# Optimization experiments

Hardware: AMD Instinct MI355X
Metric: run time of the kernel (lower is better)

The kernel has to match this reference:

```python
import jax, jax.numpy as jnp
import numpy as np

N, D, H, E = 50000, 64, 4, 400000
LN_EPS = 1e-5


def setup_inputs() -> dict:
    key = jax.random.key(0)
    ks = jax.random.split(key, 8)
    x = jax.random.normal(ks[0], (N, D), dtype=jnp.float32)
    edge_index = jax.random.randint(ks[1], (2, E), 0, N, dtype=jnp.int64)
    # nn.Linear(dim, dim*heads, bias=False): weight shape (H*D, D)
    W_lin = jax.random.normal(ks[2], (H * D, D), dtype=jnp.float32) * (1.0 / np.sqrt(D))
    attn_src = jax.random.normal(ks[3], (H, D), dtype=jnp.float32) * 0.1
    attn_dst = jax.random.normal(ks[4], (H, D), dtype=jnp.float32) * 0.1
    # nn.Linear(dim*heads, dim): weight (D, H*D), bias (D,)
    W_out = jax.random.normal(ks[5], (D, H * D), dtype=jnp.float32) * (1.0 / np.sqrt(H * D))
    b_out = jnp.zeros((D,), dtype=jnp.float32)
    ln_g = jnp.ones((D,), dtype=jnp.float32)
    ln_b = jnp.zeros((D,), dtype=jnp.float32)
    return {"x": x, "edge_index": edge_index, "W_lin": W_lin,
            "attn_src": attn_src, "attn_dst": attn_dst,
            "W_out": W_out, "b_out": b_out, "ln_g": ln_g, "ln_b": ln_b}


def reference(x, edge_index, W_lin, attn_src, attn_dst, W_out, b_out, ln_g, ln_b):
    n = x.shape[0]
    i, j = edge_index[0], edge_index[1]  # dst, src node ids per edge
    xh = (x @ W_lin.T).reshape(n, H, D)                 # [N,H,D]
    # per-node attention contributions (equivalent to per-edge dot in source)
    s_dst = jnp.einsum('nhd,hd->nh', xh, attn_dst)      # [N,H]
    s_src = jnp.einsum('nhd,hd->nh', xh, attn_src)      # [N,H]
    alpha = jax.nn.leaky_relu(s_dst[i] + s_src[j], 0.2) # [E,H]
    alpha_exp = jnp.exp(alpha)                          # source uses raw exp (no max-shift)
    denom = jax.ops.segment_sum(alpha_exp, i, num_segments=n)  # [N,H]
    attn = alpha_exp / (denom[i] + 1e-9)                # [E,H]
    msg = attn[:, :, None] * xh[j]                      # [E,H,D]
    out = jax.ops.segment_sum(msg, i, num_segments=n)   # [N,H,D]
    out = out.reshape(n, H * D) @ W_out.T + b_out       # [N,D]
    y = jax.nn.elu(out) + x
    mu = jnp.mean(y, axis=-1, keepdims=True)
    var = jnp.mean(jnp.square(y - mu), axis=-1, keepdims=True)
    return (y - mu) * jax.lax.rsqrt(var + LN_EPS) * ln_g + ln_b
```

## Files before the change

kernel.cpp:

```cpp
#include <hip/hip_runtime.h>

#define N_NODES 50000
#define DIM     64
#define HEADS   4
#define NEDGES  400000
#define HD      256
#define MAXDEG  32
#define NPREP   2048
#define ZSTRIDE 264

#define USE_DOT2 1

typedef _Float16 half2v __attribute__((ext_vector_type(2)));
typedef _Float16 half4v __attribute__((ext_vector_type(4)));
typedef _Float16 half8v __attribute__((ext_vector_type(8)));
typedef float    f32x4  __attribute__((ext_vector_type(4)));

union EU { int2 i2; half4v h; };
union HU { unsigned int u; half2v h; };

__device__ __forceinline__ half2v h2cast(unsigned int u) { HU c; c.u = u; return c.h; }

#if USE_DOT2
#define DOT2(a, b, c) __builtin_amdgcn_fdot2((a), (b), (c), false)
#else
__device__ __forceinline__ float DOT2(half2v a, half2v b, float c) {
    return fmaf((float)a[1], (float)b[1], fmaf((float)a[0], (float)b[0], c));
}
#endif

__global__ __launch_bounds__(256) void k_prep(
    const float* __restrict__ x,
    const float* __restrict__ W_lin,
    const float* __restrict__ attn_src,
    const float* __restrict__ attn_dst,
    const float* __restrict__ W_out,
    const int* __restrict__ ei,
    _Float16* __restrict__ G2T,
    _Float16* __restrict__ x16,
    float* __restrict__ S,
    int* __restrict__ cnt,
    unsigned short* __restrict__ bucketJ)
{
    __shared__ float weffsh[8][68];
    const int b = blockIdx.x, t = threadIdx.x;
    const int base = b * 32;

    const size_t e0 = (size_t)base * DIM + (size_t)t * 8;
    const bool do_x = (e0 + 8 <= (size_t)N_NODES * DIM);
    float4 u = {0.f, 0.f, 0.f, 0.f}, v = {0.f, 0.f, 0.f, 0.f};
    if (do_x) {
        u = *(const float4*)(x + e0);
        v = *(const float4*)(x + e0 + 4);
    }

    for (int e = b * 256 + t; e < NEDGES; e += NPREP * 256) {
        const int i = ei[e];
        const int j = ei[NEDGES + e];
        const int slot = atomicAdd(&cnt[i], 1);
        if (slot < MAXDEG)
            bucketJ[(size_t)i * MAXDEG + slot] = (unsigned short)j;
    }

    for (int id = t; id < 512; id += 256) {
        const int sd = id >> 8, rem = id & 255, h = rem >> 6, k = rem & 63;
        const float* av = sd ? attn_dst : attn_src;
        float a0 = 0.f, a1 = 0.f, a2 = 0.f, a3 = 0.f;
#pragma unroll
        for (int d = 0; d < DIM; d += 4) {
            a0 = fmaf(av[h * DIM + d],     W_lin[(h * DIM + d)     * DIM + k], a0);
            a1 = fmaf(av[h * DIM + d + 1], W_lin[(h * DIM + d + 1) * DIM + k], a1);
            a2 = fmaf(av[h * DIM + d + 2], W_lin[(h * DIM + d + 2) * DIM + k], a2);
            a3 = fmaf(av[h * DIM + d + 3], W_lin[(h * DIM + d + 3) * DIM + k], a3);
        }
        weffsh[sd * 4 + h][k] = (a0 + a1) + (a2 + a3);
    }

    {
        const int id = b * 256 + t;
        if (id < 64 * 256) {
            const int d = id >> 8, rem = id & 255, m = rem >> 2, h = rem & 3;
            float a0 = 0.f, a1 = 0.f, a2 = 0.f, a3 = 0.f;
#pragma unroll
            for (int k = 0; k < DIM; k += 4) {
                a0 = fmaf(W_lin[(h * DIM + k)     * DIM + m], W_out[d * HD + h * DIM + k],     a0);
                a1 = fmaf(W_lin[(h * DIM + k + 1) * DIM + m], W_out[d * HD + h * DIM + k + 1], a1);
                a2 = fmaf(W_lin[(h * DIM + k + 2) * DIM + m], W_out[d * HD + h * DIM + k + 2], a2);
                a3 = fmaf(W_lin[(h * DIM + k + 3) * DIM + m], W_out[d * HD + h * DIM + k + 3], a3);
            }
            G2T[d * HD + m * 4 + h] = (_Float16)((a0 + a1) + (a2 + a3));
        }
    }
    __syncthreads();

    {
        const int ni = base + (t >> 3);
        if (ni < N_NODES) {
            const int combo = t & 7;
            const float4* xr = (const float4*)(x + (size_t)ni * DIM);
            const float4* wr = (const float4*)(weffsh[combo]);
            float a0 = 0.f, a1 = 0.f, a2 = 0.f, a3 = 0.f;
#pragma unroll
            for (int kp = 0; kp < 16; kp += 4) {
                const float4 xa = xr[kp],     wa = wr[kp];
                const float4 xb = xr[kp + 1], wb = wr[kp + 1];
                const float4 xc = xr[kp + 2], wc = wr[kp + 2];
                const float4 xd = xr[kp + 3], wd = wr[kp + 3];
                a0 = fmaf(xa.x, wa.x, a0); a0 = fmaf(xa.y, wa.y, a0);
                a0 = fmaf(xa.z, wa.z, a0); a0 = fmaf(xa.w, wa.w, a0);
                a1 = fmaf(xb.x, wb.x, a1); a1 = fmaf(xb.y, wb.y, a1);
                a1 = fmaf(xb.z, wb.z, a1); a1 = fmaf(xb.w, wb.w, a1);
                a2 = fmaf(xc.x, wc.x, a2); a2 = fmaf(xc.y, wc.y, a2);
                a2 = fmaf(xc.z, wc.z, a2); a2 = fmaf(xc.w, wc.w, a2);
                a3 = fmaf(xd.x, wd.x, a3); a3 = fmaf(xd.y, wd.y, a3);
                a3 = fmaf(xd.z, wd.z, a3); a3 = fmaf(xd.w, wd.w, a3);
            }
            S[(size_t)ni * 8 + combo] = (a0 + a1) + (a2 + a3);
        }
        if (do_x) {
            half8v hv;
            hv[0]=(_Float16)u.x; hv[1]=(_Float16)u.y; hv[2]=(_Float16)u.z; hv[3]=(_Float16)u.w;
            hv[4]=(_Float16)v.x; hv[5]=(_Float16)v.y; hv[6]=(_Float16)v.z; hv[7]=(_Float16)v.w;
            *(half8v*)(x16 + e0) = hv;
        }
    }
}

__global__ __launch_bounds__(256) void k_ga(
    const int* __restrict__ cnt,
    const unsigned short* __restrict__ bucketJ,
    const float* __restrict__ S,
    const _Float16* __restrict__ x16,
    const _Float16* __restrict__ G2T,
    const float* __restrict__ b_out,
    const float* __restrict__ ln_g,
    const float* __restrict__ ln_b,
    float* __restrict__ out)
{
    __shared__ _Float16 znsh[16 * ZSTRIDE];
    __shared__ float ysh[16][68];
    __shared__ int2  esh[16 * 32];

    const int t = threadIdx.x, wv = t >> 6, l = t & 63;
    const int n0 = blockIdx.x * 16;
    const int side = l >> 5, p = l & 31;

    const int4 degv = *(const int4*)(cnt + n0 + wv * 4);

    int Jr[4];
#pragma unroll
    for (int r = 0; r < 4; ++r)
        Jr[r] = bucketJ[(unsigned)(n0 + wv * 4 + r) * MAXDEG + p];

    float4 SDr[4];
#pragma unroll
    for (int r = 0; r < 4; ++r)
        SDr[r] = *(const float4*)(S + (unsigned)(n0 + wv * 4 + r) * 8 + 4);

    int degc[4];
    degc[0] = degv.x < MAXDEG ? degv.x : MAXDEG;
    degc[1] = degv.y < MAXDEG ? degv.y : MAXDEG;
    degc[2] = degv.z < MAXDEG ? degv.z : MAXDEG;
    degc[3] = degv.w < MAXDEG ? degv.w : MAXDEG;

#pragma unroll
    for (int r = 0; r < 4; ++r)
        Jr[r] = (p < degc[r]) ? Jr[r] : 0;

    float4 SSr[4];
#pragma unroll
    for (int r = 0; r < 4; ++r)
        SSr[r] = *(const float4*)(S + (unsigned)Jr[r] * 8);

#pragma unroll
    for (int r = 0; r < 4; ++r) {
        float u;
        u = SDr[r].x + SSr[r].x; u = u > 0.f ? u : 0.2f * u; const float e0 = __expf(u);
        u = SDr[r].y + SSr[r].y; u = u > 0.f ? u : 0.2f * u; const float e1 = __expf(u);
        u = SDr[r].z + SSr[r].z; u = u > 0.f ? u : 0.2f * u; const float e2 = __expf(u);
        u = SDr[r].w + SSr[r].w; u = u > 0.f ? u : 0.2f * u; const float e3 = __expf(u);
        EU pk;
        pk.h[0] = (_Float16)e0; pk.h[1] = (_Float16)e1;
        pk.h[2] = (_Float16)e2; pk.h[3] = (_Float16)e3;
        int2 ev = pk.i2;
        if (p >= degc[r]) { ev.x = 0; ev.y = 0; }
        if (side == 0) esh[(wv * 4 + r) * 32 + p] = ev;
    }
    __builtin_amdgcn_wave_barrier();

    struct Grp { half2v xv[4]; int2 ee[4]; };
    float za[4], zb[4], dd[4];
    const half2v one2 = h2cast(0x3C003C00u);

    auto stage_group = [&](int r, int s, Grp& g) {
        const int jb = s + side;
#pragma unroll
        for (int q = 0; q < 4; ++q) {
            const int jv = __shfl(Jr[r], jb + 2 * q, 64);
            g.xv[q] = *(const half2v*)(x16 + (unsigned)jv * DIM + (p << 1));
        }
        const int eb = (wv * 4 + r) * 32 + jb;
#pragma unroll
        for (int q = 0; q < 4; ++q)
            g.ee[q] = esh[eb + 2 * q];
    };

    auto consume_group = [&](const Grp& g) {
#pragma unroll
        for (int pp = 0; pp < 2; ++pp) {
            const int2 ea = g.ee[2 * pp], eb2 = g.ee[2 * pp + 1];
            HU xa, xb; xa.h = g.xv[2 * pp]; xb.h = g.xv[2 * pp + 1];
            const unsigned E0 = __builtin_amdgcn_perm(eb2.x, ea.x, 0x05040100u);
            const unsigned E1 = __builtin_amdgcn_perm(eb2.x, ea.x, 0x07060302u);
            const unsigned E2 = __builtin_amdgcn_perm(eb2.y, ea.y, 0x05040100u);
            const unsigned E3 = __builtin_amdgcn_perm(eb2.y, ea.y, 0x07060302u);
            const unsigned XA = __builtin_amdgcn_perm(xb.u, xa.u, 0x05040100u);
            const unsigned XB = __builtin_amdgcn_perm(xb.u, xa.u, 0x07060302u);
            const half2v f0 = h2cast(E0), f1 = h2cast(E1);
            const half2v f2 = h2cast(E2), f3 = h2cast(E3);
            const half2v va = h2cast(XA), vb = h2cast(XB);
            za[0] = DOT2(f0, va, za[0]); za[1] = DOT2(f1, va, za[1]);
            za[2] = DOT2(f2, va, za[2]); za[3] = DOT2(f3, va, za[3]);
            zb[0] = DOT2(f0, vb, zb[0]); zb[1] = DOT2(f1, vb, zb[1]);
            zb[2] = DOT2(f2, vb, zb[2]); zb[3] = DOT2(f3, vb, zb[3]);
            dd[0] = DOT2(f0, one2, dd[0]); dd[1] = DOT2(f1, one2, dd[1]);
            dd[2] = DOT2(f2, one2, dd[2]); dd[3] = DOT2(f3, one2, dd[3]);
        }
    };

    Grp cur, nxt, remb;
    stage_group(0, 0, cur);

#pragma unroll
    for (int r = 0; r < 4; ++r) {
        const bool rem = degc[r] > 8;
        if (rem) stage_group(r, 8, remb);
        if (r < 3) stage_group(r + 1, 0, nxt);

#pragma unroll
        for (int h = 0; h < 4; ++h) { za[h] = 0.f; zb[h] = 0.f; dd[h] = 0.f; }

        consume_group(cur);
        if (rem) {
            consume_group(remb);
            for (int s = 16; s < degc[r]; s += 8) {
                Grp tg;
                stage_group(r, s, tg);
                consume_group(tg);
            }
        }

#pragma unroll
        for (int h = 0; h < 4; ++h) {
            dd[h] += __shfl_xor(dd[h], 32, 64);
            za[h] += __shfl_xor(za[h], 32, 64);
            zb[h] += __shfl_xor(zb[h], 32, 64);
        }
        const float r0 = __builtin_amdgcn_rcpf(dd[0] + 1e-9f);
        const float r1 = __builtin_amdgcn_rcpf(dd[1] + 1e-9f);
        const float r2 = __builtin_amdgcn_rcpf(dd[2] + 1e-9f);
        const float r3 = __builtin_amdgcn_rcpf(dd[3] + 1e-9f);
        if (side == 0) {
            half8v o;
            o[0] = (_Float16)(za[0] * r0); o[1] = (_Float16)(za[1] * r1);
            o[2] = (_Float16)(za[2] * r2); o[3] = (_Float16)(za[3] * r3);
            o[4] = (_Float16)(zb[0] * r0); o[5] = (_Float16)(zb[1] * r1);
            o[6] = (_Float16)(zb[2] * r2); o[7] = (_Float16)(zb[3] * r3);
            *(half8v*)(znsh + (wv * 4 + r) * ZSTRIDE + p * 8) = o;
        }
        cur = nxt;
    }
    __syncthreads();

    const int mrow = l & 15, quad = l >> 4;
    half8v A[8];
    const _Float16* zr = znsh + mrow * ZSTRIDE + quad * 8;
#pragma unroll
    for (int s = 0; s < 8; ++s)
        A[s] = *(const half8v*)(zr + 32 * s);

    const _Float16* gp = G2T + (size_t)(wv * 16 + mrow) * HD + quad * 8;
    f32x4 c0 = {0.f, 0.f, 0.f, 0.f}, c1 = {0.f, 0.f, 0.f, 0.f};
#pragma unroll
    for (int s = 0; s < 4; ++s)
        c0 = __builtin_amdgcn_mfma_f32_16x16x32_f16(A[s], *(const half8v*)(gp + 32 * s), c0, 0, 0, 0);
#pragma unroll
    for (int s = 4; s < 8; ++s)
        c1 = __builtin_amdgcn_mfma_f32_16x16x32_f16(A[s], *(const half8v*)(gp + 32 * s), c1, 0, 0, 0);
    const f32x4 c = c0 + c1;

    const int col = wv * 16 + mrow;
    const float bo = b_out[col];
#pragma unroll
    for (int rho = 0; rho < 4; ++rho) {
        const int nl = quad * 4 + rho;
        const float o = c[rho] + bo;
        const float eo = o > 0.f ? o : expm1f(o);
        ysh[nl][col] = eo + (float)x16[(size_t)(n0 + nl) * DIM + col];
    }
    __syncthreads();

    {
        const int g = l >> 4, c4 = (l & 15) * 4;
        const int nl = wv * 4 + g;
        const float4 yv = *(const float4*)(&ysh[nl][c4]);
        float s1 = (yv.x + yv.y) + (yv.z + yv.w);
        float s2 = fmaf(yv.x, yv.x, fmaf(yv.y, yv.y, fmaf(yv.z, yv.z, yv.w * yv.w)));
#pragma unroll
        for (int off = 8; off > 0; off >>= 1) {
            s1 += __shfl_xor(s1, off, 64);
            s2 += __shfl_xor(s2, off, 64);
        }
        const float mu = s1 * (1.f / 64.f);
        const float var = fmaf(-mu, mu, s2 * (1.f / 64.f));
        const float rr = rsqrtf(var + 1e-5f);
        const float4 gv = *(const float4*)(ln_g + c4);
        const float4 bv = *(const float4*)(ln_b + c4);
        float4 ov;
        ov.x = (yv.x - mu) * rr * gv.x + bv.x;
        ov.y = (yv.y - mu) * rr * gv.y + bv.y;
        ov.z = (yv.z - mu) * rr * gv.z + bv.z;
        ov.w = (yv.w - mu) * rr * gv.w + bv.w;
        *(float4*)(out + (size_t)(n0 + nl) * DIM + c4) = ov;
    }
}

extern "C" void kernel_launch(void* const* d_in, const int* in_sizes, int n_in,
                              void* d_out, int out_size, void* d_ws, size_t ws_size,
                              hipStream_t stream)
{
    const float* x        = (const float*)d_in[0];
    const int*   ei       = (const int*)d_in[1];
    const float* W_lin    = (const float*)d_in[2];
    const float* attn_src = (const float*)d_in[3];
    const float* attn_dst = (const float*)d_in[4];
    const float* W_out    = (const float*)d_in[5];
    const float* b_out    = (const float*)d_in[6];
    const float* ln_g     = (const float*)d_in[7];
    const float* ln_b     = (const float*)d_in[8];
    float* out = (float*)d_out;

    char* ws = (char*)d_ws;
    _Float16*       x16    = (_Float16*)ws;
    float*          S      = (float*)(x16 + (size_t)N_NODES * DIM);
    _Float16*       G2T    = (_Float16*)(S + (size_t)N_NODES * 8);
    int*            cnt    = (int*)(G2T + 64 * HD);
    unsigned short* bucketJ= (unsigned short*)(cnt + N_NODES);

    hipMemsetAsync(cnt, 0, (size_t)N_NODES * sizeof(int), stream);

    k_prep<<<NPREP, 256, 0, stream>>>(x, W_lin, attn_src, attn_dst, W_out, ei,
                                      G2T, x16, S, cnt, bucketJ);

    k_ga<<<N_NODES / 16, 256, 0, stream>>>(cnt, bucketJ, S, x16, G2T,
                                           b_out, ln_g, ln_b, out);
}
```

Before: 147.9 us.

## Quantize gathered node features to int8 with per-row scales folded into edge weights

Stores x as int8 with a per-node fp16 scale instead of fp16, halving the bytes read in the random neighbour gather. The per-source scale is folded into the edge weight, and the softmax denominator is computed once by a wave reduction into shared memory instead of extra dot2 accumulations. The residual now reads fp32 x directly. This adds int8-to-half conversions in the inner loop and introduces quantization error in the aggregated messages.

```diff
diff --git a/kernel.cpp b/kernel.cpp
--- a/kernel.cpp
+++ b/kernel.cpp
@@ -37,7 +37,8 @@
     const float* __restrict__ W_out,
     const int* __restrict__ ei,
     _Float16* __restrict__ G2T,
-    _Float16* __restrict__ x16,
+    signed char* __restrict__ x8,
+    _Float16* __restrict__ xscale,
     float* __restrict__ S,
     int* __restrict__ cnt,
     unsigned short* __restrict__ bucketJ)
@@ -118,10 +119,23 @@
             S[(size_t)ni * 8 + combo] = (a0 + a1) + (a2 + a3);
         }
         if (do_x) {
-            half8v hv;
-            hv[0]=(_Float16)u.x; hv[1]=(_Float16)u.y; hv[2]=(_Float16)u.z; hv[3]=(_Float16)u.w;
-            hv[4]=(_Float16)v.x; hv[5]=(_Float16)v.y; hv[6]=(_Float16)v.z; hv[7]=(_Float16)v.w;
-            *(half8v*)(x16 + e0) = hv;
+            float m0 = fabsf(u.x);
+            m0 = fmaxf(m0, fabsf(u.y)); m0 = fmaxf(m0, fabsf(u.z)); m0 = fmaxf(m0, fabsf(u.w));
+            m0 = fmaxf(m0, fabsf(v.x)); m0 = fmaxf(m0, fabsf(v.y)); m0 = fmaxf(m0, fabsf(v.z)); m0 = fmaxf(m0, fabsf(v.w));
+            m0 = fmaxf(m0, __shfl_xor(m0, 1, 64));
+            m0 = fmaxf(m0, __shfl_xor(m0, 2, 64));
+            m0 = fmaxf(m0, __shfl_xor(m0, 4, 64));
+            const float inv = m0 > 0.f ? 127.f / m0 : 0.f;
+            const int q0 = (int)rintf(u.x * inv), q1 = (int)rintf(u.y * inv);
+            const int q2 = (int)rintf(u.z * inv), q3 = (int)rintf(u.w * inv);
+            const int q4 = (int)rintf(v.x * inv), q5 = (int)rintf(v.y * inv);
+            const int q6 = (int)rintf(v.z * inv), q7 = (int)rintf(v.w * inv);
+            uint2 pk;
+            pk.x = (q0 & 255) | ((q1 & 255) << 8) | ((q2 & 255) << 16) | ((unsigned)q3 << 24);
+            pk.y = (q4 & 255) | ((q5 & 255) << 8) | ((q6 & 255) << 16) | ((unsigned)q7 << 24);
+            *(uint2*)(x8 + e0) = pk;
+            if ((t & 7) == 0)
+                xscale[base + (t >> 3)] = (_Float16)(m0 * (1.f / 127.f));
         }
     }
 }
@@ -130,7 +144,9 @@
     const int* __restrict__ cnt,
     const unsigned short* __restrict__ bucketJ,
     const float* __restrict__ S,
-    const _Float16* __restrict__ x16,
+    const signed char* __restrict__ x8,
+    const _Float16* __restrict__ xscale,
+    const float* __restrict__ x,
     const _Float16* __restrict__ G2T,
     const float* __restrict__ b_out,
     const float* __restrict__ ln_g,
@@ -140,6 +156,7 @@
     __shared__ _Float16 znsh[16 * ZSTRIDE];
     __shared__ float ysh[16][68];
     __shared__ int2  esh[16 * 32];
+    __shared__ float dsh[16][4];
 
     const int t = threadIdx.x, wv = t >> 6, l = t & 63;
     const int n0 = blockIdx.x * 16;
@@ -172,32 +189,50 @@
     for (int r = 0; r < 4; ++r)
         SSr[r] = *(const float4*)(S + (unsigned)Jr[r] * 8);
 
+    float SCr[4];
+#pragma unroll
+    for (int r = 0; r < 4; ++r)
+        SCr[r] = (float)xscale[Jr[r]];
+
 #pragma unroll
     for (int r = 0; r < 4; ++r) {
-        float u;
-        u = SDr[r].x + SSr[r].x; u = u > 0.f ? u : 0.2f * u; const float e0 = __expf(u);
-        u = SDr[r].y + SSr[r].y; u = u > 0.f ? u : 0.2f * u; const float e1 = __expf(u);
-        u = SDr[r].z + SSr[r].z; u = u > 0.f ? u : 0.2f * u; const float e2 = __expf(u);
-        u = SDr[r].w + SSr[r].w; u = u > 0.f ? u : 0.2f * u; const float e3 = __expf(u);
+        float u2;
+        u2 = SDr[r].x + SSr[r].x; u2 = u2 > 0.f ? u2 : 0.2f * u2; float e0 = __expf(u2);
+        u2 = SDr[r].y + SSr[r].y; u2 = u2 > 0.f ? u2 : 0.2f * u2; float e1 = __expf(u2);
+        u2 = SDr[r].z + SSr[r].z; u2 = u2 > 0.f ? u2 : 0.2f * u2; float e2 = __expf(u2);
+        u2 = SDr[r].w + SSr[r].w; u2 = u2 > 0.f ? u2 : 0.2f * u2; float e3 = __expf(u2);
+        if (p >= degc[r]) { e0 = 0.f; e1 = 0.f; e2 = 0.f; e3 = 0.f; }
+
+        float d0 = e0, d1 = e1, d2 = e2, d3 = e3;
+#pragma unroll
+        for (int m = 1; m < 32; m <<= 1) {
+            d0 += __shfl_xor(d0, m, 64);
+            d1 += __shfl_xor(d1, m, 64);
+            d2 += __shfl_xor(d2, m, 64);
+            d3 += __shfl_xor(d3, m, 64);
+        }
+        if (l == 0) {
+            dsh[wv * 4 + r][0] = d0; dsh[wv * 4 + r][1] = d1;
+            dsh[wv * 4 + r][2] = d2; dsh[wv * 4 + r][3] = d3;
+        }
+
+        const float sc = SCr[r];
         EU pk;
-        pk.h[0] = (_Float16)e0; pk.h[1] = (_Float16)e1;
-        pk.h[2] = (_Float16)e2; pk.h[3] = (_Float16)e3;
-        int2 ev = pk.i2;
-        if (p >= degc[r]) { ev.x = 0; ev.y = 0; }
-        if (side == 0) esh[(wv * 4 + r) * 32 + p] = ev;
+        pk.h[0] = (_Float16)(e0 * sc); pk.h[1] = (_Float16)(e1 * sc);
+        pk.h[2] = (_Float16)(e2 * sc); pk.h[3] = (_Float16)(e3 * sc);
+        if (side == 0) esh[(wv * 4 + r) * 32 + p] = pk.i2;
     }
     __builtin_amdgcn_wave_barrier();
 
-    struct Grp { half2v xv[4]; int2 ee[4]; };
-    float za[4], zb[4], dd[4];
-    const half2v one2 = h2cast(0x3C003C00u);
+    struct Grp { unsigned short xq[4]; int2 ee[4]; };
+    float za[4], zb[4];
 
     auto stage_group = [&](int r, int s, Grp& g) {
         const int jb = s + side;
 #pragma unroll
         for (int q = 0; q < 4; ++q) {
             const int jv = __shfl(Jr[r], jb + 2 * q, 64);
-            g.xv[q] = *(const half2v*)(x16 + (unsigned)jv * DIM + (p << 1));
+            g.xq[q] = *(const unsigned short*)(x8 + (unsigned)jv * DIM + (p << 1));
         }
         const int eb = (wv * 4 + r) * 32 + jb;
 #pragma unroll
@@ -209,22 +244,24 @@
 #pragma unroll
         for (int pp = 0; pp < 2; ++pp) {
             const int2 ea = g.ee[2 * pp], eb2 = g.ee[2 * pp + 1];
-            HU xa, xb; xa.h = g.xv[2 * pp]; xb.h = g.xv[2 * pp + 1];
             const unsigned E0 = __builtin_amdgcn_perm(eb2.x, ea.x, 0x05040100u);
             const unsigned E1 = __builtin_amdgcn_perm(eb2.x, ea.x, 0x07060302u);
             const unsigned E2 = __builtin_amdgcn_perm(eb2.y, ea.y, 0x05040100u);
             const unsigned E3 = __builtin_amdgcn_perm(eb2.y, ea.y, 0x07060302u);
-            const unsigned XA = __builtin_amdgcn_perm(xb.u, xa.u, 0x05040100u);
-            const unsigned XB = __builtin_amdgcn_perm(xb.u, xa.u, 0x07060302u);
+            const int ua = g.xq[2 * pp], ub = g.xq[2 * pp + 1];
+            const float fa0 = (float)(signed char)(ua & 255);
+            const float fa1 = (float)(signed char)(ua >> 8);
+            const float fb0 = (float)(signed char)(ub & 255);
+            const float fb1 = (float)(signed char)(ub >> 8);
+            half2v va, vb;
+            va[0] = (_Float16)fa0; va[1] = (_Float16)fb0;
+            vb[0] = (_Float16)fa1; vb[1] = (_Float16)fb1;
             const half2v f0 = h2cast(E0), f1 = h2cast(E1);
             const half2v f2 = h2cast(E2), f3 = h2cast(E3);
-            const half2v va = h2cast(XA), vb = h2cast(XB);
             za[0] = DOT2(f0, va, za[0]); za[1] = DOT2(f1, va, za[1]);
             za[2] = DOT2(f2, va, za[2]); za[3] = DOT2(f3, va, za[3]);
             zb[0] = DOT2(f0, vb, zb[0]); zb[1] = DOT2(f1, vb, zb[1]);
             zb[2] = DOT2(f2, vb, zb[2]); zb[3] = DOT2(f3, vb, zb[3]);
-            dd[0] = DOT2(f0, one2, dd[0]); dd[1] = DOT2(f1, one2, dd[1]);
-            dd[2] = DOT2(f2, one2, dd[2]); dd[3] = DOT2(f3, one2, dd[3]);
         }
     };
 
@@ -238,7 +275,7 @@
         if (r < 3) stage_group(r + 1, 0, nxt);
 
 #pragma unroll
-        for (int h = 0; h < 4; ++h) { za[h] = 0.f; zb[h] = 0.f; dd[h] = 0.f; }
+        for (int h = 0; h < 4; ++h) { za[h] = 0.f; zb[h] = 0.f; }
 
         consume_group(cur);
         if (rem) {
@@ -252,15 +289,15 @@
 
 #pragma unroll
         for (int h = 0; h < 4; ++h) {
-            dd[h] += __shfl_xor(dd[h], 32, 64);
             za[h] += __shfl_xor(za[h], 32, 64);
             zb[h] += __shfl_xor(zb[h], 32, 64);
         }
-        const float r0 = __builtin_amdgcn_rcpf(dd[0] + 1e-9f);
-        const float r1 = __builtin_amdgcn_rcpf(dd[1] + 1e-9f);
-        const float r2 = __builtin_amdgcn_rcpf(dd[2] + 1e-9f);
-        const float r3 = __builtin_amdgcn_rcpf(dd[3] + 1e-9f);
         if (side == 0) {
+            const float4 dv = *(const float4*)(dsh[wv * 4 + r]);
+            const float r0 = __builtin_amdgcn_rcpf(dv.x + 1e-9f);
+            const float r1 = __builtin_amdgcn_rcpf(dv.y + 1e-9f);
+            const float r2 = __builtin_amdgcn_rcpf(dv.z + 1e-9f);
+            const float r3 = __builtin_amdgcn_rcpf(dv.w + 1e-9f);
             half8v o;
             o[0] = (_Float16)(za[0] * r0); o[1] = (_Float16)(za[1] * r1);
             o[2] = (_Float16)(za[2] * r2); o[3] = (_Float16)(za[3] * r3);
@@ -296,7 +333,7 @@
         const int nl = quad * 4 + rho;
         const float o = c[rho] + bo;
         const float eo = o > 0.f ? o : expm1f(o);
-        ysh[nl][col] = eo + (float)x16[(size_t)(n0 + nl) * DIM + col];
+        ysh[nl][col] = eo + x[(size_t)(n0 + nl) * DIM + col];
     }
     __syncthreads();
 
@@ -341,8 +378,9 @@
     float* out = (float*)d_out;
 
     char* ws = (char*)d_ws;
-    _Float16*       x16    = (_Float16*)ws;
-    float*          S      = (float*)(x16 + (size_t)N_NODES * DIM);
+    signed char*    x8     = (signed char*)ws;
+    _Float16*       xscale = (_Float16*)(x8 + (size_t)N_NODES * DIM);
+    float*          S      = (float*)(xscale + N_NODES);
     _Float16*       G2T    = (_Float16*)(S + (size_t)N_NODES * 8);
     int*            cnt    = (int*)(G2T + 64 * HD);
     unsigned short* bucketJ= (unsigned short*)(cnt + N_NODES);
@@ -350,8 +388,8 @@
     hipMemsetAsync(cnt, 0, (size_t)N_NODES * sizeof(int), stream);
 
     k_prep<<<NPREP, 256, 0, stream>>>(x, W_lin, attn_src, attn_dst, W_out, ei,
-                                      G2T, x16, S, cnt, bucketJ);
-
-    k_ga<<<N_NODES / 16, 256, 0, stream>>>(cnt, bucketJ, S, x16, G2T,
+                                      G2T, x8, xscale, S, cnt, bucketJ);
+
+    k_ga<<<N_NODES / 16, 256, 0, stream>>>(cnt, bucketJ, S, x8, xscale, x, G2T,
                                            b_out, ln_g, ln_b, out);
 }
```

After: 154.2 us. 1.04x slower.
